# Kernel tuning notes

Hardware: AMD Instinct MI355X
Metric: run time of the kernel (lower is better)

The kernel has to match this reference:

```python
import jax, jax.numpy as jnp
import numpy as np

NODE_DIM = 128
EDGE_DIM = 128
N_NODES = 10000
N_EDGES = 640000


def setup_inputs() -> dict:
    key = jax.random.key(0)
    ks = jax.random.split(key, 11)
    x = jax.random.normal(ks[0], (N_NODES, NODE_DIM), dtype=jnp.float32)
    edge_index = jax.random.randint(ks[1], (2, N_EDGES), 0, N_NODES, dtype=jnp.int32)
    edge_attr = jax.random.normal(ks[2], (N_EDGES, EDGE_DIM), dtype=jnp.float32)

    def lin(k, fan_in, fan_out):
        kw, kb = jax.random.split(k)
        bound = 1.0 / np.sqrt(fan_in)
        W = jax.random.uniform(kw, (fan_in, fan_out), minval=-bound, maxval=bound, dtype=jnp.float32)
        b = jax.random.uniform(kb, (fan_out,), minval=-bound, maxval=bound, dtype=jnp.float32)
        return W, b

    # node_update: Linear(node+edge -> node), Softplus, Linear(node -> node)
    nW1, nb1 = lin(ks[3], NODE_DIM + EDGE_DIM, NODE_DIM)
    nW2, nb2 = lin(ks[4], NODE_DIM, NODE_DIM)
    # edge_update_net: Linear(2*node+edge -> edge), Softplus, Linear(edge -> edge)
    eW1, eb1 = lin(ks[5], 2 * NODE_DIM + EDGE_DIM, EDGE_DIM)
    eW2, eb2 = lin(ks[6], EDGE_DIM, EDGE_DIM)

    return {
        "x": x, "edge_index": edge_index, "edge_attr": edge_attr,
        "nW1": nW1, "nb1": nb1, "nW2": nW2, "nb2": nb2,
        "eW1": eW1, "eb1": eb1, "eW2": eW2, "eb2": eb2,
    }


def reference(x, edge_index, edge_attr, nW1, nb1, nW2, nb2, eW1, eb1, eW2, eb2):
    row, col = edge_index[0], edge_index[1]
    x_row = x[row]              # [E, node_dim]
    x_col = x[col]              # [E, node_dim]

    # edge update MLP
    edge_input = jnp.concatenate([x_row, x_col, edge_attr], axis=1)  # [E, 2n+e]
    h = jax.nn.softplus(edge_input @ eW1 + eb1)
    edge_attr_new = h @ eW2 + eb2                                     # [E, edge_dim]

    # node message MLP
    msg_in = jnp.concatenate([x_row, edge_attr_new], axis=1)          # [E, n+e]
    m = jax.nn.softplus(msg_in @ nW1 + nb1)
    messages = m @ nW2 + nb2                                          # [E, node_dim]

    # scatter_add messages into destination nodes (col)
    x_new = jax.ops.segment_sum(messages, col, num_segments=x.shape[0])
    return (x_new, edge_attr_new)
```

## Files before the change

### kernel.cpp

```cpp
#include <hip/hip_runtime.h>
#include <cstdint>

#define N_NODES   10000
#define N_EDGES   640000
#define NODE_OUT  (N_NODES * 128)

typedef __bf16 bf16;
typedef bf16  bf16x8 __attribute__((ext_vector_type(8)));
typedef float f32x4  __attribute__((ext_vector_type(4)));

#define EW1T_OFF 0
#define EW2T_OFF 49152
#define NW1T_OFF 65536
#define NW2T_OFF 98304
#define XB_OFF   114688
#define WS_NEED_BYTES (229376 + 2560000)

__global__ void transpose_weights(const float* __restrict__ eW1, const float* __restrict__ eW2,
                                  const float* __restrict__ nW1, const float* __restrict__ nW2,
                                  bf16* __restrict__ wt) {
  int gid = blockIdx.x * 256 + threadIdx.x;
  const float* src; bf16* dst; int K, off;
  if (gid < 49152)      { src = eW1; dst = wt + EW1T_OFF; K = 384; off = gid; }
  else if (gid < 65536) { src = eW2; dst = wt + EW2T_OFF; K = 128; off = gid - 49152; }
  else if (gid < 98304) { src = nW1; dst = wt + NW1T_OFF; K = 256; off = gid - 65536; }
  else                  { src = nW2; dst = wt + NW2T_OFF; K = 128; off = gid - 98304; }
  int k = off >> 7, n = off & 127;
  dst[n * K + k] = (bf16)src[off];
}

__device__ __forceinline__ float softplus_f(float v) {
  return v > 20.f ? v : __logf(1.f + __expf(v));
}

__device__ __forceinline__ bf16x8 cvt8(float4 f0, float4 f1) {
  bf16x8 h;
  h[0] = (bf16)f0.x; h[1] = (bf16)f0.y; h[2] = (bf16)f0.z; h[3] = (bf16)f0.w;
  h[4] = (bf16)f1.x; h[5] = (bf16)f1.y; h[6] = (bf16)f1.z; h[7] = (bf16)f1.w;
  return h;
}

__device__ __forceinline__ bf16x8 load_cvt8(const float* __restrict__ src) {
  float4 f0 = *(const float4*)src;
  float4 f1 = *(const float4*)(src + 4);
  return cvt8(f0, f1);
}

__global__ void convert_x(const float* __restrict__ x, bf16* __restrict__ xb) {
  int i = (blockIdx.x * 256 + threadIdx.x) * 8;
  *(bf16x8*)&xb[i] = load_cvt8(x + i);
}

template<bool XB>
__global__ void __launch_bounds__(256, 2)
edge_mlp(const float* __restrict__ x, const bf16* __restrict__ xb,
         const int* __restrict__ eidx, const float* __restrict__ edge_attr,
         const float* __restrict__ eb1, const float* __restrict__ eb2,
         const bf16* __restrict__ wt, float* __restrict__ edge_out)
{
  __shared__ bf16 sA[32 * 384];
  __shared__ bf16 sC[32 * 128];

  const int tid  = threadIdx.x;
  const int wave = tid >> 6, lane = tid & 63;
  const int ln15 = lane & 15, lq = lane >> 4;
  const int n0 = wave * 32;
  const int sw = ln15 & 7;

  bf16x8 w1[12][2], w2[4][2];
  #pragma unroll
  for (int c = 0; c < 12; ++c)
    #pragma unroll
    for (int t = 0; t < 2; ++t)
      w1[c][t] = *(const bf16x8*)&wt[EW1T_OFF + (n0 + t * 16 + ln15) * 384 + c * 32 + lq * 8];
  #pragma unroll
  for (int c = 0; c < 4; ++c)
    #pragma unroll
    for (int t = 0; t < 2; ++t)
      w2[c][t] = *(const bf16x8*)&wt[EW2T_OFF + (n0 + t * 16 + ln15) * 128 + c * 32 + lq * 8];
  float b1[2], b2[2];
  #pragma unroll
  for (int t = 0; t < 2; ++t) {
    b1[t] = eb1[n0 + t * 16 + ln15];
    b2[t] = eb2[n0 + t * 16 + ln15];
  }

  const int eA = tid >> 4, eB = eA + 16;
  const int pl = tid & 15, lp = pl ^ (eA & 7);

  uint4  hx0, hx1, hc0, hc1;
  float4 px0[2], px1[2], pc0[2], pc1[2];
  float4 pa0[2], pa1[2];

  const int NT = N_EDGES / 32;

  {
    const int e0 = blockIdx.x * 32;
    int riA = eidx[e0 + eA], riB = eidx[e0 + eB];
    int ciA = eidx[N_EDGES + e0 + eA], ciB = eidx[N_EDGES + e0 + eB];
    if constexpr (XB) {
      hx0 = *(const uint4*)&xb[(size_t)riA * 128 + lp * 8];
      hx1 = *(const uint4*)&xb[(size_t)riB * 128 + lp * 8];
      hc0 = *(const uint4*)&xb[(size_t)ciA * 128 + lp * 8];
      hc1 = *(const uint4*)&xb[(size_t)ciB * 128 + lp * 8];
    } else {
      px0[0] = *(const float4*)(x + (size_t)riA * 128 + lp * 8);
      px0[1] = *(const float4*)(x + (size_t)riA * 128 + lp * 8 + 4);
      px1[0] = *(const float4*)(x + (size_t)riB * 128 + lp * 8);
      px1[1] = *(const float4*)(x + (size_t)riB * 128 + lp * 8 + 4);
      pc0[0] = *(const float4*)(x + (size_t)ciA * 128 + lp * 8);
      pc0[1] = *(const float4*)(x + (size_t)ciA * 128 + lp * 8 + 4);
      pc1[0] = *(const float4*)(x + (size_t)ciB * 128 + lp * 8);
      pc1[1] = *(const float4*)(x + (size_t)ciB * 128 + lp * 8 + 4);
    }
    pa0[0] = *(const float4*)(edge_attr + (size_t)(e0 + eA) * 128 + lp * 8);
    pa0[1] = *(const float4*)(edge_attr + (size_t)(e0 + eA) * 128 + lp * 8 + 4);
    pa1[0] = *(const float4*)(edge_attr + (size_t)(e0 + eB) * 128 + lp * 8);
    pa1[1] = *(const float4*)(edge_attr + (size_t)(e0 + eB) * 128 + lp * 8 + 4);
  }

  for (int tile = blockIdx.x; tile < NT; tile += gridDim.x) {
    const int e0 = tile * 32;

    if constexpr (XB) {
      *(uint4*)&sA[eA * 384 + (0 * 16 + pl) * 8] = hx0;
      *(uint4*)&sA[eB * 384 + (0 * 16 + pl) * 8] = hx1;
      *(uint4*)&sA[eA * 384 + (1 * 16 + pl) * 8] = hc0;
      *(uint4*)&sA[eB * 384 + (1 * 16 + pl) * 8] = hc1;
    } else {
      *(bf16x8*)&sA[eA * 384 + (0 * 16 + pl) * 8] = cvt8(px0[0], px0[1]);
      *(bf16x8*)&sA[eB * 384 + (0 * 16 + pl) * 8] = cvt8(px1[0], px1[1]);
      *(bf16x8*)&sA[eA * 384 + (1 * 16 + pl) * 8] = cvt8(pc0[0], pc0[1]);
      *(bf16x8*)&sA[eB * 384 + (1 * 16 + pl) * 8] = cvt8(pc1[0], pc1[1]);
    }
    *(bf16x8*)&sA[eA * 384 + (2 * 16 + pl) * 8] = cvt8(pa0[0], pa0[1]);
    *(bf16x8*)&sA[eB * 384 + (2 * 16 + pl) * 8] = cvt8(pa1[0], pa1[1]);

    const int tn = tile + gridDim.x;
    if (tn < NT) {
      const int en = tn * 32;
      int riA = eidx[en + eA], riB = eidx[en + eB];
      int ciA = eidx[N_EDGES + en + eA], ciB = eidx[N_EDGES + en + eB];
      if constexpr (XB) {
        hx0 = *(const uint4*)&xb[(size_t)riA * 128 + lp * 8];
        hx1 = *(const uint4*)&xb[(size_t)riB * 128 + lp * 8];
        hc0 = *(const uint4*)&xb[(size_t)ciA * 128 + lp * 8];
        hc1 = *(const uint4*)&xb[(size_t)ciB * 128 + lp * 8];
      } else {
        px0[0] = *(const float4*)(x + (size_t)riA * 128 + lp * 8);
        px0[1] = *(const float4*)(x + (size_t)riA * 128 + lp * 8 + 4);
        px1[0] = *(const float4*)(x + (size_t)riB * 128 + lp * 8);
        px1[1] = *(const float4*)(x + (size_t)riB * 128 + lp * 8 + 4);
        pc0[0] = *(const float4*)(x + (size_t)ciA * 128 + lp * 8);
        pc0[1] = *(const float4*)(x + (size_t)ciA * 128 + lp * 8 + 4);
        pc1[0] = *(const float4*)(x + (size_t)ciB * 128 + lp * 8);
        pc1[1] = *(const float4*)(x + (size_t)ciB * 128 + lp * 8 + 4);
      }
      pa0[0] = *(const float4*)(edge_attr + (size_t)(en + eA) * 128 + lp * 8);
      pa0[1] = *(const float4*)(edge_attr + (size_t)(en + eA) * 128 + lp * 8 + 4);
      pa1[0] = *(const float4*)(edge_attr + (size_t)(en + eB) * 128 + lp * 8);
      pa1[1] = *(const float4*)(edge_attr + (size_t)(en + eB) * 128 + lp * 8 + 4);
    }
    __syncthreads();

    f32x4 acc[2][2];
    #pragma unroll
    for (int mf = 0; mf < 2; ++mf)
      #pragma unroll
      for (int t = 0; t < 2; ++t)
        acc[mf][t] = f32x4{0.f, 0.f, 0.f, 0.f};
    #pragma unroll
    for (int c = 0; c < 12; ++c) {
      int s = (((c * 4 + lq) ^ sw) << 3);
      bf16x8 a0 = *(const bf16x8*)&sA[ln15 * 384 + s];
      bf16x8 a1 = *(const bf16x8*)&sA[(16 + ln15) * 384 + s];
      #pragma unroll
      for (int t = 0; t < 2; ++t) {
        acc[0][t] = __builtin_amdgcn_mfma_f32_16x16x32_bf16(a0, w1[c][t], acc[0][t], 0, 0, 0);
        acc[1][t] = __builtin_amdgcn_mfma_f32_16x16x32_bf16(a1, w1[c][t], acc[1][t], 0, 0, 0);
      }
    }

    #pragma unroll
    for (int mf = 0; mf < 2; ++mf)
      #pragma unroll
      for (int t = 0; t < 2; ++t)
        #pragma unroll
        for (int r = 0; r < 4; ++r) {
          float v = softplus_f(acc[mf][t][r] + b1[t]);
          int row = mf * 16 + lq * 4 + r;
          int col = n0 + t * 16 + ln15;
          sC[row * 128 + ((((col >> 3) ^ (row & 7))) << 3) + (col & 7)] = (bf16)v;
        }
    __syncthreads();

    f32x4 d[2][2];
    #pragma unroll
    for (int mf = 0; mf < 2; ++mf)
      #pragma unroll
      for (int t = 0; t < 2; ++t)
        d[mf][t] = f32x4{0.f, 0.f, 0.f, 0.f};
    #pragma unroll
    for (int c = 0; c < 4; ++c) {
      int s = (((c * 4 + lq) ^ sw) << 3);
      bf16x8 a0 = *(const bf16x8*)&sC[ln15 * 128 + s];
      bf16x8 a1 = *(const bf16x8*)&sC[(16 + ln15) * 128 + s];
      #pragma unroll
      for (int t = 0; t < 2; ++t) {
        d[0][t] = __builtin_amdgcn_mfma_f32_16x16x32_bf16(a0, w2[c][t], d[0][t], 0, 0, 0);
        d[1][t] = __builtin_amdgcn_mfma_f32_16x16x32_bf16(a1, w2[c][t], d[1][t], 0, 0, 0);
      }
    }
    #pragma unroll
    for (int mf = 0; mf < 2; ++mf)
      #pragma unroll
      for (int t = 0; t < 2; ++t)
        #pragma unroll
        for (int r = 0; r < 4; ++r) {
          int row = mf * 16 + lq * 4 + r;
          edge_out[(size_t)(e0 + row) * 128 + n0 + t * 16 + ln15] = d[mf][t][r] + b2[t];
        }
  }
}

template<bool XB>
__global__ void __launch_bounds__(256, 2)
node_mlp(const float* __restrict__ x, const bf16* __restrict__ xb,
         const int* __restrict__ eidx, const float* __restrict__ edge_new,
         const float* __restrict__ nb1, const float* __restrict__ nb2,
         const bf16* __restrict__ wt, float* __restrict__ node_out)
{
  __shared__ bf16 sA[32 * 384];

  const int tid  = threadIdx.x;
  const int wave = tid >> 6, lane = tid & 63;
  const int ln15 = lane & 15, lq = lane >> 4;
  const int n0 = wave * 32;
  const int sw = ln15 & 7;

  bf16x8 w3[8][2], w4[4][2];
  #pragma unroll
  for (int c = 0; c < 8; ++c)
    #pragma unroll
    for (int t = 0; t < 2; ++t)
      w3[c][t] = *(const bf16x8*)&wt[NW1T_OFF + (n0 + t * 16 + ln15) * 256 + c * 32 + lq * 8];
  #pragma unroll
  for (int c = 0; c < 4; ++c)
    #pragma unroll
    for (int t = 0; t < 2; ++t)
      w4[c][t] = *(const bf16x8*)&wt[NW2T_OFF + (n0 + t * 16 + ln15) * 128 + c * 32 + lq * 8];
  float b3[2], b4[2];
  #pragma unroll
  for (int t = 0; t < 2; ++t) {
    b3[t] = nb1[n0 + t * 16 + ln15];
    b4[t] = nb2[n0 + t * 16 + ln15];
  }

  const int eA = tid >> 4, eB = eA + 16;
  const int pl = tid & 15, lp = pl ^ (eA & 7);

  uint4  hx0, hx1;
  float4 px0[2], px1[2];
  float4 pe0[2], pe1[2];

  const int NT = N_EDGES / 32;

  {
    const int e0 = blockIdx.x * 32;
    int riA = eidx[e0 + eA], riB = eidx[e0 + eB];
    if constexpr (XB) {
      hx0 = *(const uint4*)&xb[(size_t)riA * 128 + lp * 8];
      hx1 = *(const uint4*)&xb[(size_t)riB * 128 + lp * 8];
    } else {
      px0[0] = *(const float4*)(x + (size_t)riA * 128 + lp * 8);
      px0[1] = *(const float4*)(x + (size_t)riA * 128 + lp * 8 + 4);
      px1[0] = *(const float4*)(x + (size_t)riB * 128 + lp * 8);
      px1[1] = *(const float4*)(x + (size_t)riB * 128 + lp * 8 + 4);
    }
    pe0[0] = *(const float4*)(edge_new + (size_t)(e0 + eA) * 128 + lp * 8);
    pe0[1] = *(const float4*)(edge_new + (size_t)(e0 + eA) * 128 + lp * 8 + 4);
    pe1[0] = *(const float4*)(edge_new + (size_t)(e0 + eB) * 128 + lp * 8);
    pe1[1] = *(const float4*)(edge_new + (size_t)(e0 + eB) * 128 + lp * 8 + 4);
  }

  for (int tile = blockIdx.x; tile < NT; tile += gridDim.x) {
    const int e0 = tile * 32;

    if constexpr (XB) {
      *(uint4*)&sA[eA * 384 + (0 * 16 + pl) * 8] = hx0;
      *(uint4*)&sA[eB * 384 + (0 * 16 + pl) * 8] = hx1;
    } else {
      *(bf16x8*)&sA[eA * 384 + (0 * 16 + pl) * 8] = cvt8(px0[0], px0[1]);
      *(bf16x8*)&sA[eB * 384 + (0 * 16 + pl) * 8] = cvt8(px1[0], px1[1]);
    }
    *(bf16x8*)&sA[eA * 384 + (1 * 16 + pl) * 8] = cvt8(pe0[0], pe0[1]);
    *(bf16x8*)&sA[eB * 384 + (1 * 16 + pl) * 8] = cvt8(pe1[0], pe1[1]);

    const int tn = tile + gridDim.x;
    if (tn < NT) {
      const int en = tn * 32;
      int riA = eidx[en + eA], riB = eidx[en + eB];
      if constexpr (XB) {
        hx0 = *(const uint4*)&xb[(size_t)riA * 128 + lp * 8];
        hx1 = *(const uint4*)&xb[(size_t)riB * 128 + lp * 8];
      } else {
        px0[0] = *(const float4*)(x + (size_t)riA * 128 + lp * 8);
        px0[1] = *(const float4*)(x + (size_t)riA * 128 + lp * 8 + 4);
        px1[0] = *(const float4*)(x + (size_t)riB * 128 + lp * 8);
        px1[1] = *(const float4*)(x + (size_t)riB * 128 + lp * 8 + 4);
      }
      pe0[0] = *(const float4*)(edge_new + (size_t)(en + eA) * 128 + lp * 8);
      pe0[1] = *(const float4*)(edge_new + (size_t)(en + eA) * 128 + lp * 8 + 4);
      pe1[0] = *(const float4*)(edge_new + (size_t)(en + eB) * 128 + lp * 8);
      pe1[1] = *(const float4*)(edge_new + (size_t)(en + eB) * 128 + lp * 8 + 4);
    }
    __syncthreads();

    f32x4 acc[2][2];
    #pragma unroll
    for (int mf = 0; mf < 2; ++mf)
      #pragma unroll
      for (int t = 0; t < 2; ++t)
        acc[mf][t] = f32x4{0.f, 0.f, 0.f, 0.f};
    #pragma unroll
    for (int c = 0; c < 8; ++c) {
      int s = (((c * 4 + lq) ^ sw) << 3);
      bf16x8 a0 = *(const bf16x8*)&sA[ln15 * 384 + s];
      bf16x8 a1 = *(const bf16x8*)&sA[(16 + ln15) * 384 + s];
      #pragma unroll
      for (int t = 0; t < 2; ++t) {
        acc[0][t] = __builtin_amdgcn_mfma_f32_16x16x32_bf16(a0, w3[c][t], acc[0][t], 0, 0, 0);
        acc[1][t] = __builtin_amdgcn_mfma_f32_16x16x32_bf16(a1, w3[c][t], acc[1][t], 0, 0, 0);
      }
    }

    #pragma unroll
    for (int mf = 0; mf < 2; ++mf)
      #pragma unroll
      for (int t = 0; t < 2; ++t)
        #pragma unroll
        for (int r = 0; r < 4; ++r) {
          float v = softplus_f(acc[mf][t][r] + b3[t]);
          int row = mf * 16 + lq * 4 + r;
          int col = n0 + t * 16 + ln15;
          int ls  = 32 + (col >> 3);
          sA[row * 384 + ((ls ^ (row & 7)) << 3) + (col & 7)] = (bf16)v;
        }
    __syncthreads();

    f32x4 d[2][2];
    #pragma unroll
    for (int mf = 0; mf < 2; ++mf)
      #pragma unroll
      for (int t = 0; t < 2; ++t)
        d[mf][t] = f32x4{0.f, 0.f, 0.f, 0.f};
    #pragma unroll
    for (int c = 0; c < 4; ++c) {
      int s = (((32 + c * 4 + lq) ^ sw) << 3);
      bf16x8 a0 = *(const bf16x8*)&sA[ln15 * 384 + s];
      bf16x8 a1 = *(const bf16x8*)&sA[(16 + ln15) * 384 + s];
      #pragma unroll
      for (int t = 0; t < 2; ++t) {
        d[0][t] = __builtin_amdgcn_mfma_f32_16x16x32_bf16(a0, w4[c][t], d[0][t], 0, 0, 0);
        d[1][t] = __builtin_amdgcn_mfma_f32_16x16x32_bf16(a1, w4[c][t], d[1][t], 0, 0, 0);
      }
    }
    #pragma unroll
    for (int mf = 0; mf < 2; ++mf) {
      int4 q = *(const int4*)&eidx[N_EDGES + e0 + mf * 16 + lq * 4];
      int nid[4] = {q.x, q.y, q.z, q.w};
      #pragma unroll
      for (int t = 0; t < 2; ++t) {
        int col = n0 + t * 16 + ln15;
        #pragma unroll
        for (int r = 0; r < 4; ++r) {
          float v = d[mf][t][r] + b4[t];
          unsafeAtomicAdd(&node_out[(size_t)nid[r] * 128 + col], v);
        }
      }
    }
  }
}

extern "C" void kernel_launch(void* const* d_in, const int* in_sizes, int n_in,
                              void* d_out, int out_size, void* d_ws, size_t ws_size,
                              hipStream_t stream) {
  const float* x    = (const float*)d_in[0];
  const int*   eidx = (const int*)d_in[1];
  const float* ea   = (const float*)d_in[2];
  const float* nW1  = (const float*)d_in[3];
  const float* nb1  = (const float*)d_in[4];
  const float* nW2  = (const float*)d_in[5];
  const float* nb2  = (const float*)d_in[6];
  const float* eW1  = (const float*)d_in[7];
  const float* eb1  = (const float*)d_in[8];
  const float* eW2  = (const float*)d_in[9];
  const float* eb2  = (const float*)d_in[10];

  bf16*  wt        = (bf16*)d_ws;
  float* out_nodes = (float*)d_out;
  float* out_edges = out_nodes + NODE_OUT;

  hipMemsetAsync(out_nodes, 0, NODE_OUT * sizeof(float), stream);
  transpose_weights<<<448, 256, 0, stream>>>(eW1, eW2, nW1, nW2, wt);

  const bool use_xb = ws_size >= (size_t)WS_NEED_BYTES;
  bf16* xb = wt + XB_OFF;
  if (use_xb) {
    convert_x<<<625, 256, 0, stream>>>(x, xb);
    edge_mlp<true><<<512, 256, 0, stream>>>(x, xb, eidx, ea, eb1, eb2, wt, out_edges);
    node_mlp<true><<<512, 256, 0, stream>>>(x, xb, eidx, out_edges, nb1, nb2, wt, out_nodes);
  } else {
    edge_mlp<false><<<512, 256, 0, stream>>>(x, nullptr, eidx, ea, eb1, eb2, wt, out_edges);
    node_mlp<false><<<512, 256, 0, stream>>>(x, nullptr, eidx, out_edges, nb1, nb2, wt, out_nodes);
  }
}
```

Measured before the change: 839.2 us.

## Sort edges by destination node to pre-reduce messages before atomic scatter

Adds a counting sort of edges by destination node (histogram, single-block scan, scatter into a permutation). The node MLP then walks edges in sorted order and reduces runs of same-destination rows in registers or with wave shuffles before issuing atomics. The goal is fewer contended global float atomics in the scatter-add. In exchange it adds three small kernels plus a memset, and the gathers of edge features become permuted (non-coalesced) reads. It also requires more workspace, and if that is not available the old path runs.

```diff
diff --git a/kernel.cpp b/kernel.cpp
--- a/kernel.cpp
+++ b/kernel.cpp
@@ -14,7 +14,11 @@
 #define NW1T_OFF 65536
 #define NW2T_OFF 98304
 #define XB_OFF   114688
-#define WS_NEED_BYTES (229376 + 2560000)
+#define WS_XB_BYTES    (229376 + 2560000)
+#define CUR_BYTE_OFF   WS_XB_BYTES
+#define PERM_BYTE_OFF  (CUR_BYTE_OFF + 40064)
+#define CSORT_BYTE_OFF (PERM_BYTE_OFF + 2560000)
+#define WS_SORT_BYTES  (CSORT_BYTE_OFF + 2560000)
 
 __global__ void transpose_weights(const float* __restrict__ eW1, const float* __restrict__ eW2,
                                   const float* __restrict__ nW1, const float* __restrict__ nW2,
@@ -49,6 +53,40 @@
 __global__ void convert_x(const float* __restrict__ x, bf16* __restrict__ xb) {
   int i = (blockIdx.x * 256 + threadIdx.x) * 8;
   *(bf16x8*)&xb[i] = load_cvt8(x + i);
+}
+
+__global__ void hist_k(const int* __restrict__ eidx, int* __restrict__ hist) {
+  int g = blockIdx.x * 256 + threadIdx.x;
+  atomicAdd(&hist[eidx[N_EDGES + g]], 1);
+}
+
+__global__ void scan_k(int* __restrict__ cur) {
+  __shared__ int part[1024];
+  int tid = threadIdx.x;
+  int base = tid * 10;
+  int loc[10]; int s = 0;
+  #pragma unroll
+  for (int i = 0; i < 10; ++i) {
+    int v = (base + i < N_NODES) ? cur[base + i] : 0;
+    loc[i] = s; s += v;
+  }
+  part[tid] = s; __syncthreads();
+  for (int off = 1; off < 1024; off <<= 1) {
+    int v = (tid >= off) ? part[tid - off] : 0;
+    __syncthreads(); part[tid] += v; __syncthreads();
+  }
+  int pre = tid ? part[tid - 1] : 0;
+  #pragma unroll
+  for (int i = 0; i < 10; ++i)
+    if (base + i < N_NODES) cur[base + i] = pre + loc[i];
+}
+
+__global__ void scatter_k(const int* __restrict__ eidx, int* __restrict__ cur,
+                          int* __restrict__ perm, int* __restrict__ csort) {
+  int g = blockIdx.x * 256 + threadIdx.x;
+  int c = eidx[N_EDGES + g];
+  int p = atomicAdd(&cur[c], 1);
+  perm[p] = g; csort[p] = c;
 }
 
 template<bool XB>
@@ -223,10 +261,11 @@
   }
 }
 
-template<bool XB>
+template<bool XB, bool SORTED>
 __global__ void __launch_bounds__(256, 2)
 node_mlp(const float* __restrict__ x, const bf16* __restrict__ xb,
          const int* __restrict__ eidx, const float* __restrict__ edge_new,
+         const int* __restrict__ perm, const int* __restrict__ csort,
          const float* __restrict__ nb1, const float* __restrict__ nb2,
          const bf16* __restrict__ wt, float* __restrict__ node_out)
 {
@@ -267,7 +306,10 @@
 
   {
     const int e0 = blockIdx.x * 32;
-    int riA = eidx[e0 + eA], riB = eidx[e0 + eB];
+    int epA, epB;
+    if constexpr (SORTED) { epA = perm[e0 + eA]; epB = perm[e0 + eB]; }
+    else                  { epA = e0 + eA;       epB = e0 + eB; }
+    int riA = eidx[epA], riB = eidx[epB];
     if constexpr (XB) {
       hx0 = *(const uint4*)&xb[(size_t)riA * 128 + lp * 8];
       hx1 = *(const uint4*)&xb[(size_t)riB * 128 + lp * 8];
@@ -277,10 +319,10 @@
       px1[0] = *(const float4*)(x + (size_t)riB * 128 + lp * 8);
       px1[1] = *(const float4*)(x + (size_t)riB * 128 + lp * 8 + 4);
     }
-    pe0[0] = *(const float4*)(edge_new + (size_t)(e0 + eA) * 128 + lp * 8);
-    pe0[1] = *(const float4*)(edge_new + (size_t)(e0 + eA) * 128 + lp * 8 + 4);
-    pe1[0] = *(const float4*)(edge_new + (size_t)(e0 + eB) * 128 + lp * 8);
-    pe1[1] = *(const float4*)(edge_new + (size_t)(e0 + eB) * 128 + lp * 8 + 4);
+    pe0[0] = *(const float4*)(edge_new + (size_t)epA * 128 + lp * 8);
+    pe0[1] = *(const float4*)(edge_new + (size_t)epA * 128 + lp * 8 + 4);
+    pe1[0] = *(const float4*)(edge_new + (size_t)epB * 128 + lp * 8);
+    pe1[1] = *(const float4*)(edge_new + (size_t)epB * 128 + lp * 8 + 4);
   }
 
   for (int tile = blockIdx.x; tile < NT; tile += gridDim.x) {
@@ -299,7 +341,10 @@
     const int tn = tile + gridDim.x;
     if (tn < NT) {
       const int en = tn * 32;
-      int riA = eidx[en + eA], riB = eidx[en + eB];
+      int epA, epB;
+      if constexpr (SORTED) { epA = perm[en + eA]; epB = perm[en + eB]; }
+      else                  { epA = en + eA;       epB = en + eB; }
+      int riA = eidx[epA], riB = eidx[epB];
       if constexpr (XB) {
         hx0 = *(const uint4*)&xb[(size_t)riA * 128 + lp * 8];
         hx1 = *(const uint4*)&xb[(size_t)riB * 128 + lp * 8];
@@ -309,10 +354,10 @@
         px1[0] = *(const float4*)(x + (size_t)riB * 128 + lp * 8);
         px1[1] = *(const float4*)(x + (size_t)riB * 128 + lp * 8 + 4);
       }
-      pe0[0] = *(const float4*)(edge_new + (size_t)(en + eA) * 128 + lp * 8);
-      pe0[1] = *(const float4*)(edge_new + (size_t)(en + eA) * 128 + lp * 8 + 4);
-      pe1[0] = *(const float4*)(edge_new + (size_t)(en + eB) * 128 + lp * 8);
-      pe1[1] = *(const float4*)(edge_new + (size_t)(en + eB) * 128 + lp * 8 + 4);
+      pe0[0] = *(const float4*)(edge_new + (size_t)epA * 128 + lp * 8);
+      pe0[1] = *(const float4*)(edge_new + (size_t)epA * 128 + lp * 8 + 4);
+      pe1[0] = *(const float4*)(edge_new + (size_t)epB * 128 + lp * 8);
+      pe1[1] = *(const float4*)(edge_new + (size_t)epB * 128 + lp * 8 + 4);
     }
     __syncthreads();
 
@@ -365,17 +410,54 @@
         d[1][t] = __builtin_amdgcn_mfma_f32_16x16x32_bf16(a1, w4[c][t], d[1][t], 0, 0, 0);
       }
     }
-    #pragma unroll
-    for (int mf = 0; mf < 2; ++mf) {
-      int4 q = *(const int4*)&eidx[N_EDGES + e0 + mf * 16 + lq * 4];
-      int nid[4] = {q.x, q.y, q.z, q.w};
-      #pragma unroll
-      for (int t = 0; t < 2; ++t) {
-        int col = n0 + t * 16 + ln15;
+
+    if constexpr (SORTED) {
+      #pragma unroll
+      for (int mf = 0; mf < 2; ++mf) {
+        int4 q = *(const int4*)&csort[e0 + mf * 16 + lq * 4];
+        int nid[4] = {q.x, q.y, q.z, q.w};
+        bool all4 = (nid[0] == nid[1]) && (nid[1] == nid[2]) && (nid[2] == nid[3]);
+        int first0 = __shfl(nid[0], ln15);
+        bool uni = __all(all4 && (nid[0] == first0));
         #pragma unroll
-        for (int r = 0; r < 4; ++r) {
-          float v = d[mf][t][r] + b4[t];
-          unsafeAtomicAdd(&node_out[(size_t)nid[r] * 128 + col], v);
+        for (int t = 0; t < 2; ++t) {
+          int col = n0 + t * 16 + ln15;
+          float v[4];
+          #pragma unroll
+          for (int r = 0; r < 4; ++r) v[r] = d[mf][t][r] + b4[t];
+          if (uni) {
+            float s = (v[0] + v[1]) + (v[2] + v[3]);
+            s += __shfl_xor(s, 16);
+            s += __shfl_xor(s, 32);
+            if (lq == 0)
+              unsafeAtomicAdd(&node_out[(size_t)nid[0] * 128 + col], s);
+          } else {
+            float s = v[0]; int curn = nid[0];
+            #pragma unroll
+            for (int r = 1; r < 4; ++r) {
+              if (nid[r] == curn) s += v[r];
+              else {
+                unsafeAtomicAdd(&node_out[(size_t)curn * 128 + col], s);
+                curn = nid[r]; s = v[r];
+              }
+            }
+            unsafeAtomicAdd(&node_out[(size_t)curn * 128 + col], s);
+          }
+        }
+      }
+    } else {
+      #pragma unroll
+      for (int mf = 0; mf < 2; ++mf) {
+        int4 q = *(const int4*)&eidx[N_EDGES + e0 + mf * 16 + lq * 4];
+        int nid[4] = {q.x, q.y, q.z, q.w};
+        #pragma unroll
+        for (int t = 0; t < 2; ++t) {
+          int col = n0 + t * 16 + ln15;
+          #pragma unroll
+          for (int r = 0; r < 4; ++r) {
+            float v = d[mf][t][r] + b4[t];
+            unsafeAtomicAdd(&node_out[(size_t)nid[r] * 128 + col], v);
+          }
         }
       }
     }
@@ -404,14 +486,30 @@
   hipMemsetAsync(out_nodes, 0, NODE_OUT * sizeof(float), stream);
   transpose_weights<<<448, 256, 0, stream>>>(eW1, eW2, nW1, nW2, wt);
 
-  const bool use_xb = ws_size >= (size_t)WS_NEED_BYTES;
-  bf16* xb = wt + XB_OFF;
-  if (use_xb) {
+  const bool use_xb   = ws_size >= (size_t)WS_XB_BYTES;
+  const bool use_sort = ws_size >= (size_t)WS_SORT_BYTES;
+  bf16* xb   = wt + XB_OFF;
+  int* cur   = (int*)((char*)d_ws + CUR_BYTE_OFF);
+  int* perm  = (int*)((char*)d_ws + PERM_BYTE_OFF);
+  int* csort = (int*)((char*)d_ws + CSORT_BYTE_OFF);
+
+  if (use_sort) {
+    convert_x<<<625, 256, 0, stream>>>(x, xb);
+    hipMemsetAsync(cur, 0, N_NODES * sizeof(int), stream);
+    hist_k<<<2500, 256, 0, stream>>>(eidx, cur);
+    scan_k<<<1, 1024, 0, stream>>>(cur);
+    scatter_k<<<2500, 256, 0, stream>>>(eidx, cur, perm, csort);
+    edge_mlp<true><<<512, 256, 0, stream>>>(x, xb, eidx, ea, eb1, eb2, wt, out_edges);
+    node_mlp<true, true><<<512, 256, 0, stream>>>(x, xb, eidx, out_edges, perm, csort,
+                                                  nb1, nb2, wt, out_nodes);
+  } else if (use_xb) {
     convert_x<<<625, 256, 0, stream>>>(x, xb);
     edge_mlp<true><<<512, 256, 0, stream>>>(x, xb, eidx, ea, eb1, eb2, wt, out_edges);
-    node_mlp<true><<<512, 256, 0, stream>>>(x, xb, eidx, out_edges, nb1, nb2, wt, out_nodes);
+    node_mlp<true, false><<<512, 256, 0, stream>>>(x, xb, eidx, out_edges, nullptr, nullptr,
+                                                   nb1, nb2, wt, out_nodes);
   } else {
     edge_mlp<false><<<512, 256, 0, stream>>>(x, nullptr, eidx, ea, eb1, eb2, wt, out_edges);
-    node_mlp<false><<<512, 256, 0, stream>>>(x, nullptr, eidx, out_edges, nb1, nb2, wt, out_nodes);
-  }
-}
+    node_mlp<false, false><<<512, 256, 0, stream>>>(x, nullptr, eidx, out_edges, nullptr, nullptr,
+                                                    nb1, nb2, wt, out_nodes);
+  }
+}
```

New measurement: 834.3 us. Within noise of the previous version (-0.6%).
